# Optimization experiments

Hardware: AMD Instinct MI355X
Metric: run time of the kernel (lower is better)

The kernel has to match this reference:

```python
import jax, jax.numpy as jnp
import numpy as np

HOP = 256
B, F, NB = 16, 4096, 65

def setup_inputs() -> dict:
    key = jax.random.key(0)
    k1, k2 = jax.random.split(key)
    filter_bank = jax.random.normal(k1, (B, F, NB), dtype=jnp.float32)
    noise_u = jax.random.uniform(k2, (B, F, HOP), dtype=jnp.float32)
    return {"filter_bank": filter_bank, "noise_u": noise_u}

def amp_to_impulse_response(amp, target_size):
    # treat real amp as complex spectrum with zero imag, go to time domain
    amp_c = jax.lax.complex(amp, jnp.zeros_like(amp))
    ir = jnp.fft.irfft(amp_c, axis=-1)            # [B, F, 2*(NB-1)]
    filter_size = ir.shape[-1]
    ir = jnp.roll(ir, filter_size // 2, axis=-1)
    n = jnp.arange(filter_size, dtype=ir.dtype)
    win = 0.5 * (1.0 - jnp.cos(2.0 * jnp.pi * n / filter_size))  # periodic hann (torch default)
    ir = ir * win
    ir = jnp.pad(ir, ((0, 0), (0, 0), (0, target_size - filter_size)))
    ir = jnp.roll(ir, -(filter_size // 2), axis=-1)
    return ir

def fft_convolve(signal, kernel):
    n = signal.shape[-1]
    sig = jnp.pad(signal, ((0, 0), (0, 0), (0, n)))
    ker = jnp.pad(kernel, ((0, 0), (0, 0), (kernel.shape[-1], 0)))
    out = jnp.fft.irfft(jnp.fft.rfft(sig) * jnp.fft.rfft(ker))
    return out[..., out.shape[-1] // 2:]

def reference(filter_bank, noise_u):
    impulse = amp_to_impulse_response(filter_bank, HOP)   # [B, F, HOP]
    noise = noise_u * 2.0 - 1.0                           # [B, F, HOP]
    out = fft_convolve(noise, impulse)                    # [B, F, HOP]
    return out.reshape(out.shape[0], -1, 1)               # [B, F*HOP, 1]
```

## Files before the change

kernel.cpp:

```cpp
#include <hip/hip_runtime.h>
#include <math.h>

#define NB 65
#define HOPS 256
#define RPB 8
#define THREADS 128
#define TAPS_OFF 360
#define RSTRIDE 492

#define PHYS(i) ((i) + (((i) >> 5) << 2))

__device__ __forceinline__ void load16(float (&d)[16], const float* p) {
#pragma unroll
    for (int x = 0; x < 4; ++x) {
        float4 v = *(const float4*)(p + 4 * x);
        d[4*x] = v.x; d[4*x+1] = v.y; d[4*x+2] = v.z; d[4*x+3] = v.w;
    }
}
__device__ __forceinline__ void load16s(float (&d)[16], const float* rowbuf, int L) {
#pragma unroll
    for (int x = 0; x < 4; ++x) {
        float4 v = *(const float4*)(rowbuf + PHYS(L + 4 * x));
        d[4*x] = v.x; d[4*x+1] = v.y; d[4*x+2] = v.z; d[4*x+3] = v.w;
    }
}
__device__ __forceinline__ void fma16(float (&f)[16], const float (&tp)[16],
                                      const float (&lo)[16], const float (&hi)[16]) {
#pragma unroll
    for (int kk = 0; kk < 16; ++kk) {
        float t = tp[kk];
#pragma unroll
        for (int d = 0; d < 16; ++d) {
            int j = 16 + d - kk;
            f[d] = fmaf(t, (j < 16) ? lo[j] : hi[j - 16], f[d]);
        }
    }
}

__global__ __launch_bounds__(THREADS, 4) void noisefilter_kernel(
    const float* __restrict__ fb,
    const float* __restrict__ nz,
    float* __restrict__ out)
{
    __shared__ float lds[RPB * RSTRIDE];
    const int tid = threadIdx.x;
    const int r   = tid >> 4;
    const int l16 = tid & 15;
    const int t0  = l16 << 4;
    const size_t row0 = (size_t)blockIdx.x * RPB;
    float* rowbuf = &lds[r * RSTRIDE];

    const float* fbb = fb + row0 * NB;
    for (int i = tid; i < RPB * NB; i += THREADS) {
        int rr = i / NB;
        int k  = i - rr * NB;
        lds[rr * RSTRIDE + TAPS_OFF + k] = fbb[i];
    }

    const float4* nz4 = (const float4*)(nz + row0 * HOPS);
    float4 nv[4];
#pragma unroll
    for (int p = 0; p < 4; ++p) nv[p] = nz4[tid + p * THREADS];

    __syncthreads();

    const float alphaA = (float)l16 * 0.04908738521234052f;
    const float alphaB = alphaA + 0.7853981633974483f;
    const float cA = __cosf(alphaA), cB = __cosf(alphaB);
    const float c2A = fmaf(2.0f * cA, cA, -1.0f);
    const float c2B = fmaf(2.0f * cB, cB, -1.0f);
    const float k2A = c2A + c2A, k2B = c2B + c2B;

    float eA1=0.f,eA2=0.f,oA1=0.f,oA2=0.f;
    float eB1=0.f,eB2=0.f,oB1=0.f,oB2=0.f;
    float s32 = 0.f, a0r = 0.f, a64r;

    const float* amp = rowbuf + TAPS_OFF;
    {
        float a = amp[64];
        a64r = a;
        { float t = a - eA2; float s = fmaf(k2A, eA1, t); eA2 = eA1; eA1 = s; }
        { float t = a - eB2; float s = fmaf(k2B, eB1, t); eB2 = eB1; eB1 = s; }
        s32 += a;
    }
#pragma unroll
    for (int kb = 48; kb >= 0; kb -= 16) {
        float ab[16];
        load16(ab, amp + kb);
#pragma unroll
        for (int kk = 15; kk >= 0; --kk) {
            float a = ab[kk];
            if (kk & 1) {
                { float t = a - oA2; float s = fmaf(k2A, oA1, t); oA2 = oA1; oA1 = s; }
                { float t = a - oB2; float s = fmaf(k2B, oB1, t); oB2 = oB1; oB1 = s; }
            } else {
                { float t = a - eA2; float s = fmaf(k2A, eA1, t); eA2 = eA1; eA1 = s; }
                { float t = a - eB2; float s = fmaf(k2B, eB1, t); eB2 = eB1; eB1 = s; }
                if ((kk >> 1) & 1) s32 -= a; else s32 += a;
            }
        }
        if (kb == 0) a0r = ab[0];
    }

    const float EA = fmaf(-c2A, eA2, eA1);
    const float OA = cA * (oA1 - oA2);
    const float EB = fmaf(-c2B, eB2, eB1);
    const float OB = cB * (oB1 - oB2);
    const float pm = (l16 & 1) ? -1.f : 1.f;
    const float corr = fmaf(pm, a64r, a0r);
    const float inv = 1.0f / 256.0f;
    float* tps = rowbuf + TAPS_OFF;

    {
        float GA  = fmaf(2.f, EA + OA, -corr);
        float GAm = fmaf(2.f, EA - OA, -corr);
        float TA  = GA  * (1.0f + cA) * inv;
        float TAm = GAm * (1.0f - cA) * inv;
        tps[l16] = TA;
        tps[64 - l16] = TAm;
        if (l16 >= 1) { tps[128 - l16] = TA; tps[64 + l16] = TAm; }
    }
    {
        float GB  = fmaf(2.f, EB + OB, -corr);
        float GBm = fmaf(2.f, EB - OB, -corr);
        float TB  = GB  * (1.0f + cB) * inv;
        float TBm = GBm * (1.0f - cB) * inv;
        tps[16 + l16] = TB;  tps[112 - l16] = TB;
        tps[48 - l16] = TBm; tps[80 + l16]  = TBm;
    }
    {
        float G32 = fmaf(2.f, s32, -(a0r + a64r));
        float T32 = G32 * inv;
        tps[32] = T32;
        tps[96] = T32;
    }

    *(float4*)(rowbuf + PHYS(4 * l16)) = make_float4(0.f, 0.f, 0.f, 0.f);

#pragma unroll
    for (int p = 0; p < 4; ++p) {
        int idx = tid + p * THREADS;
        float4 v = nv[p];
        int rr = idx >> 6;
        int o  = ((idx & 63) << 2) + 64;
        *(float4*)(&lds[rr * RSTRIDE + PHYS(o)]) =
            make_float4(fmaf(2.f, v.x, -1.f), fmaf(2.f, v.y, -1.f),
                        fmaf(2.f, v.z, -1.f), fmaf(2.f, v.w, -1.f));
    }
    __syncthreads();

    float f[16];
#pragma unroll
    for (int d = 0; d < 16; ++d) f[d] = 0.f;
    float X[16], Y[16], Z[16], tp[16];
    {
        const int b0 = t0 + 48;
        load16s(X, rowbuf, b0);      load16s(Y, rowbuf, b0 + 16);
        load16(tp, tps + 0);   fma16(f, tp, X, Y);
        load16s(Z, rowbuf, b0 - 16);
        load16(tp, tps + 16);  fma16(f, tp, Z, X);
        load16s(Y, rowbuf, b0 - 32);
        load16(tp, tps + 32);  fma16(f, tp, Y, Z);
        load16s(X, rowbuf, b0 - 48);
        load16(tp, tps + 48);  fma16(f, tp, X, Y);
    }

    float g[4] = {0.f, 0.f, 0.f, 0.f};
#pragma unroll
    for (int c = 0; c < 4; ++c) {
        float W[20];
#pragma unroll
        for (int x = 0; x < 5; ++x) {
            float4 v = *(const float4*)(rowbuf + PHYS(48 + 4 * l16 - 16 * c + 4 * x));
            W[4*x] = v.x; W[4*x+1] = v.y; W[4*x+2] = v.z; W[4*x+3] = v.w;
        }
        float tp2[16];
        load16(tp2, tps + 64 + 16 * c);
#pragma unroll
        for (int kk = 0; kk < 16; ++kk) {
            float t = tp2[kk];
#pragma unroll
            for (int d = 0; d < 4; ++d)
                g[d] = fmaf(t, W[16 + d - kk], g[d]);
        }
    }
    *(float4*)(tps + 64 + 4 * l16) = make_float4(g[0], g[1], g[2], g[3]);
    if (l16 >= 12) {
        const float* sc = tps + 64 + ((l16 - 12) << 4);
#pragma unroll
        for (int x = 0; x < 4; ++x) {
            float4 v = *(const float4*)(sc + 4 * x);
            f[4*x]   += v.x; f[4*x+1] += v.y;
            f[4*x+2] += v.z; f[4*x+3] += v.w;
        }
    }

    float* op = out + (row0 + r) * HOPS + t0;
#pragma unroll
    for (int x = 0; x < 4; ++x)
        *(float4*)(op + 4 * x) = make_float4(f[4*x], f[4*x+1], f[4*x+2], f[4*x+3]);
}

extern "C" void kernel_launch(void* const* d_in, const int* in_sizes, int n_in,
                              void* d_out, int out_size, void* d_ws, size_t ws_size,
                              hipStream_t stream) {
    const float* fb = (const float*)d_in[0];
    const float* nz = (const float*)d_in[1];
    float* o = (float*)d_out;
    const int rows = 16 * 4096;
    noisefilter_kernel<<<dim3(rows / RPB), dim3(THREADS), 0, stream>>>(fb, nz, o);
}
```

Measured before the change: 153.3 us.

## Swizzle LDS rows with XOR, halve stored taps, fuse tail convolution chunks

Replaces the padded LDS indexing with an XOR swizzle on float4 chunks, which shrinks the per-row stride. Only the first 65 taps are now written, and the symmetric upper half is read back through reversed indexing with a carry value. The second-stage partial convolution is interleaved with the main fma16 passes and skipped for lanes where it is not needed, aiming to cut LDS traffic and footprint and reuse loaded tap registers. The cost is extra index arithmetic and divergent branches in the chunk helper.

```diff
diff --git a/kernel.cpp b/kernel.cpp
--- a/kernel.cpp
+++ b/kernel.cpp
@@ -5,10 +5,13 @@
 #define HOPS 256
 #define RPB 8
 #define THREADS 128
-#define TAPS_OFF 360
-#define RSTRIDE 492
-
-#define PHYS(i) ((i) + (((i) >> 5) << 2))
+#define TAPS_OFF 320
+#define RSTRIDE 456
+
+__device__ __forceinline__ int phys4(int i) {
+    int c = i >> 2;
+    return (c ^ ((c >> 3) & 7)) << 2;
+}
 
 __device__ __forceinline__ void load16(float (&d)[16], const float* p) {
 #pragma unroll
@@ -20,7 +23,7 @@
 __device__ __forceinline__ void load16s(float (&d)[16], const float* rowbuf, int L) {
 #pragma unroll
     for (int x = 0; x < 4; ++x) {
-        float4 v = *(const float4*)(rowbuf + PHYS(L + 4 * x));
+        float4 v = *(const float4*)(rowbuf + phys4(L + 4 * x));
         d[4*x] = v.x; d[4*x+1] = v.y; d[4*x+2] = v.z; d[4*x+3] = v.w;
     }
 }
@@ -33,6 +36,25 @@
         for (int d = 0; d < 16; ++d) {
             int j = 16 + d - kk;
             f[d] = fmaf(t, (j < 16) ? lo[j] : hi[j - 16], f[d]);
+        }
+    }
+}
+template <int C>
+__device__ __forceinline__ void c2chunk(float (&g)[4], float carry, const float (&tp)[16],
+                                        const float* rowbuf, int l16) {
+    if (l16 >= 4 * C) {
+        float W[20];
+#pragma unroll
+        for (int x = 0; x < 5; ++x) {
+            float4 v = *(const float4*)(rowbuf + phys4(48 + 4 * l16 - 16 * C + 4 * x));
+            W[4*x] = v.x; W[4*x+1] = v.y; W[4*x+2] = v.z; W[4*x+3] = v.w;
+        }
+#pragma unroll
+        for (int kk = 0; kk < 16; ++kk) {
+            float t = (kk == 0) ? carry : tp[16 - kk];
+#pragma unroll
+            for (int d = 0; d < 4; ++d)
+                g[d] = fmaf(t, W[16 + d - kk], g[d]);
         }
     }
 }
@@ -114,28 +136,21 @@
     {
         float GA  = fmaf(2.f, EA + OA, -corr);
         float GAm = fmaf(2.f, EA - OA, -corr);
-        float TA  = GA  * (1.0f + cA) * inv;
-        float TAm = GAm * (1.0f - cA) * inv;
-        tps[l16] = TA;
-        tps[64 - l16] = TAm;
-        if (l16 >= 1) { tps[128 - l16] = TA; tps[64 + l16] = TAm; }
+        tps[l16]      = GA  * (1.0f + cA) * inv;
+        tps[64 - l16] = GAm * (1.0f - cA) * inv;
     }
     {
         float GB  = fmaf(2.f, EB + OB, -corr);
         float GBm = fmaf(2.f, EB - OB, -corr);
-        float TB  = GB  * (1.0f + cB) * inv;
-        float TBm = GBm * (1.0f - cB) * inv;
-        tps[16 + l16] = TB;  tps[112 - l16] = TB;
-        tps[48 - l16] = TBm; tps[80 + l16]  = TBm;
+        tps[16 + l16] = GB  * (1.0f + cB) * inv;
+        tps[48 - l16] = GBm * (1.0f - cB) * inv;
     }
     {
         float G32 = fmaf(2.f, s32, -(a0r + a64r));
-        float T32 = G32 * inv;
-        tps[32] = T32;
-        tps[96] = T32;
-    }
-
-    *(float4*)(rowbuf + PHYS(4 * l16)) = make_float4(0.f, 0.f, 0.f, 0.f);
+        tps[32] = G32 * inv;
+    }
+
+    *(float4*)(rowbuf + phys4(4 * l16)) = make_float4(0.f, 0.f, 0.f, 0.f);
 
 #pragma unroll
     for (int p = 0; p < 4; ++p) {
@@ -143,7 +158,7 @@
         float4 v = nv[p];
         int rr = idx >> 6;
         int o  = ((idx & 63) << 2) + 64;
-        *(float4*)(&lds[rr * RSTRIDE + PHYS(o)]) =
+        *(float4*)(&lds[rr * RSTRIDE + phys4(o)]) =
             make_float4(fmaf(2.f, v.x, -1.f), fmaf(2.f, v.y, -1.f),
                         fmaf(2.f, v.z, -1.f), fmaf(2.f, v.w, -1.f));
     }
@@ -152,38 +167,23 @@
     float f[16];
 #pragma unroll
     for (int d = 0; d < 16; ++d) f[d] = 0.f;
+    float g[4] = {0.f, 0.f, 0.f, 0.f};
     float X[16], Y[16], Z[16], tp[16];
-    {
-        const int b0 = t0 + 48;
-        load16s(X, rowbuf, b0);      load16s(Y, rowbuf, b0 + 16);
-        load16(tp, tps + 0);   fma16(f, tp, X, Y);
-        load16s(Z, rowbuf, b0 - 16);
-        load16(tp, tps + 16);  fma16(f, tp, Z, X);
-        load16s(Y, rowbuf, b0 - 32);
-        load16(tp, tps + 32);  fma16(f, tp, Y, Z);
-        load16s(X, rowbuf, b0 - 48);
-        load16(tp, tps + 48);  fma16(f, tp, X, Y);
-    }
-
-    float g[4] = {0.f, 0.f, 0.f, 0.f};
-#pragma unroll
-    for (int c = 0; c < 4; ++c) {
-        float W[20];
-#pragma unroll
-        for (int x = 0; x < 5; ++x) {
-            float4 v = *(const float4*)(rowbuf + PHYS(48 + 4 * l16 - 16 * c + 4 * x));
-            W[4*x] = v.x; W[4*x+1] = v.y; W[4*x+2] = v.z; W[4*x+3] = v.w;
-        }
-        float tp2[16];
-        load16(tp2, tps + 64 + 16 * c);
-#pragma unroll
-        for (int kk = 0; kk < 16; ++kk) {
-            float t = tp2[kk];
-#pragma unroll
-            for (int d = 0; d < 4; ++d)
-                g[d] = fmaf(t, W[16 + d - kk], g[d]);
-        }
-    }
+    float carry = tps[64];
+
+    load16s(X, rowbuf, t0);      load16s(Y, rowbuf, t0 + 16);
+    load16(tp, tps + 48); fma16(f, tp, X, Y);
+    c2chunk<0>(g, carry, tp, rowbuf, l16); carry = tp[0];
+    load16s(Z, rowbuf, t0 + 32);
+    load16(tp, tps + 32); fma16(f, tp, Y, Z);
+    c2chunk<1>(g, carry, tp, rowbuf, l16); carry = tp[0];
+    load16s(X, rowbuf, t0 + 48);
+    load16(tp, tps + 16); fma16(f, tp, Z, X);
+    c2chunk<2>(g, carry, tp, rowbuf, l16); carry = tp[0];
+    load16s(Y, rowbuf, t0 + 64);
+    load16(tp, tps + 0);  fma16(f, tp, X, Y);
+    c2chunk<3>(g, carry, tp, rowbuf, l16);
+
     *(float4*)(tps + 64 + 4 * l16) = make_float4(g[0], g[1], g[2], g[3]);
     if (l16 >= 12) {
         const float* sc = tps + 64 + ((l16 - 12) << 4);
```

New measurement: 320.6 us. 109% more time.
